# Kernel optimization log

Hardware: AMD Instinct MI355X
Metric: run time of the kernel (lower is better)

The kernel has to match this reference:

```python
import jax, jax.numpy as jnp
import numpy as np

HIDDEN = 512
HEADS = 8
LN_EPS = 1e-5


def setup_inputs() -> dict:
    key = jax.random.key(0)
    ks = jax.random.split(key, 10)
    n, bsz, h = 128, 4, HIDDEN
    state = jax.random.normal(ks[0], (n, n, bsz, h), dtype=jnp.float32)
    relation = jax.random.normal(ks[1], (n, n, bsz, h), dtype=jnp.float32)
    attn_mask = jnp.zeros((n, bsz, n), dtype=bool)  # key_padding_mask, True = pad
    std = 0.02
    Wq = jax.random.normal(ks[2], (h, h), dtype=jnp.float32) * std
    bq = jnp.zeros((h,), dtype=jnp.float32)
    Wk = jax.random.normal(ks[3], (h, h), dtype=jnp.float32) * std
    bk = jnp.zeros((h,), dtype=jnp.float32)
    Wp = jax.random.normal(ks[4], (h, 2 * h), dtype=jnp.float32) * std
    bp = jnp.zeros((h,), dtype=jnp.float32)
    gamma = jnp.ones((h,), dtype=jnp.float32)
    beta = jnp.zeros((h,), dtype=jnp.float32)
    return {"state": state, "relation": relation, "attn_mask": attn_mask, "n": n,
            "Wq": Wq, "bq": bq, "Wk": Wk, "bk": bk, "Wp": Wp, "bp": bp,
            "gamma": gamma, "beta": beta}


def reference(state, relation, attn_mask, n, Wq, bq, Wk, bk, Wp, bp, gamma, beta):
    # state, relation: [n, n, bsz, h]; attn_mask: [n, bsz, n] (True = pad key)
    h = state.shape[-1]
    dh = h // HEADS
    scale = dh ** -0.5
    # per-row self-attention weights (eval mode: attention dropout is identity)
    q = (jnp.einsum('itbh,oh->itbo', state, Wq) + bq) * scale
    k = jnp.einsum('isbh,oh->isbo', state, Wk) + bk
    qh = q.reshape(q.shape[0], q.shape[1], q.shape[2], HEADS, dh)
    kh = k.reshape(k.shape[0], k.shape[1], k.shape[2], HEADS, dh)
    scores = jnp.einsum('itbnd,isbnd->ibnts', qh, kh)  # [n, bsz, H, t, s]
    pad = attn_mask[:, :, None, None, :]               # [n, bsz, 1, 1, s]
    scores = jnp.where(pad, -jnp.inf, scores)
    probs = jax.nn.softmax(scores, axis=-1)
    w = probs.mean(axis=2)                             # avg over heads -> [n, bsz, t, s]
    # x[i,t,b] = sum_s w[i,b,t,s] * state[i,s,b]
    x = jnp.einsum('ibts,isbh->itbh', w, state)
    # rel_mix[i,t,b] = sum_s w[i,b,t,s] * relation[s,t,b]
    rel_mix = jnp.einsum('ibts,stbh->itbh', w, relation)
    cat = jnp.concatenate([x, rel_mix], axis=-1)       # [n, n, bsz, 2h]
    out = jax.nn.relu(jnp.einsum('itbc,hc->itbh', cat, Wp) + bp)
    # dropout is identity in eval mode; residual + layernorm
    y = state + out
    mu = y.mean(axis=-1, keepdims=True)
    var = y.var(axis=-1, keepdims=True)
    return gamma * (y - mu) * jax.lax.rsqrt(var + LN_EPS) + beta
```

## Files before the change

kernel.cpp:

```cpp
#include <hip/hip_runtime.h>

typedef unsigned short u16;
typedef __attribute__((ext_vector_type(4))) unsigned short u16x4;
typedef __attribute__((ext_vector_type(8))) unsigned short u16x8;
typedef __attribute__((ext_vector_type(8))) short bf16x8;
typedef __attribute__((ext_vector_type(4))) float f32x4;

__device__ __forceinline__ u16 f2bf(float f) {
  union { float f; unsigned u; } v; v.f = f;
  unsigned r = v.u + 0x7fffu + ((v.u >> 16) & 1u);
  return (u16)(r >> 16);
}
__device__ __forceinline__ float bf2f(u16 u) {
  union { unsigned u; float f; } v; v.u = ((unsigned)u) << 16;
  return v.f;
}
__device__ __forceinline__ void gload16(const void* g, void* l) {
  __builtin_amdgcn_global_load_lds(
      (const __attribute__((address_space(1))) unsigned int*)g,
      (__attribute__((address_space(3))) unsigned int*)l, 16, 0, 0);
}

__global__ __launch_bounds__(256) void k_prep(
    const float* __restrict__ Wq, const float* __restrict__ Wk,
    const float* __restrict__ bq, const float* __restrict__ bk,
    const float* __restrict__ Wp,
    u16* __restrict__ wqk, u16* __restrict__ wp, float* __restrict__ bqk) {
  int idx = blockIdx.x * 256 + threadIdx.x;
  if (idx < 524288) {
    int o = idx >> 9, hh = idx & 511;
    wqk[idx] = f2bf((o < 512) ? Wq[o * 512 + hh] * 0.125f : Wk[(o - 512) * 512 + hh]);
    wp[idx] = f2bf(Wp[idx]);
  }
  if (idx < 1024) bqk[idx] = (idx < 512) ? bq[idx] * 0.125f : bk[idx - 512];
}

__global__ __launch_bounds__(256) void k_transpose_state(
    const float* __restrict__ src, u16* __restrict__ dst, u16* __restrict__ stB) {
  const int i = blockIdx.z, b = blockIdx.y;
  const int s0 = (blockIdx.x & 1) * 64, h0 = (blockIdx.x >> 1) * 64;
  __shared__ u16 T[64][72];
  const int tid = threadIdx.x;
  const int ls = tid >> 4, lh = (tid & 15) * 4;
#pragma unroll
  for (int rr = 0; rr < 4; ++rr) {
    int s = rr * 16 + ls;
    size_t flat = ((size_t)(i * 128 + s0 + s) * 4 + b) * 512 + h0 + lh;
    f32x4 v = *(const f32x4*)&src[flat];
    u16x4 w4 = { f2bf(v.x), f2bf(v.y), f2bf(v.z), f2bf(v.w) };
    *(u16x4*)&T[s][lh] = w4;
    *(u16x4*)&stB[flat] = w4;
  }
  __syncthreads();
#pragma unroll
  for (int it = 0; it < 2; ++it) {
    int work = it * 256 + tid;
    int hh = work >> 3, sg = (work & 7) * 8;
    u16x8 o;
#pragma unroll
    for (int j = 0; j < 8; ++j) o[j] = T[sg + j][hh];
    *(u16x8*)&dst[((i * 4 + b) * 512 + h0 + hh) * 128 + s0 + sg] = o;
  }
}

__global__ __launch_bounds__(256) void k_transpose_rel(
    const float* __restrict__ src, u16* __restrict__ dst) {
  const int t = blockIdx.z, b = blockIdx.y;
  const int s0 = (blockIdx.x & 1) * 64, h0 = (blockIdx.x >> 1) * 64;
  __shared__ u16 T[64][72];
  const int tid = threadIdx.x;
  const int ls = tid >> 4, lh = (tid & 15) * 4;
#pragma unroll
  for (int rr = 0; rr < 4; ++rr) {
    int s = rr * 16 + ls;
    f32x4 v = *(const f32x4*)&src[(((s0 + s) * 128 + t) * 4 + b) * 512 + h0 + lh];
    u16x4 w4 = { f2bf(v.x), f2bf(v.y), f2bf(v.z), f2bf(v.w) };
    *(u16x4*)&T[s][lh] = w4;
  }
  __syncthreads();
#pragma unroll
  for (int it = 0; it < 2; ++it) {
    int work = it * 256 + tid;
    int hh = work >> 3, sg = (work & 7) * 8;
    u16x8 o;
#pragma unroll
    for (int j = 0; j < 8; ++j) o[j] = T[sg + j][hh];
    *(u16x8*)&dst[((t * 4 + b) * 512 + h0 + hh) * 128 + s0 + sg] = o;
  }
}

__global__ __launch_bounds__(256) void k_qkproj(
    const u16* __restrict__ stB, const u16* __restrict__ wqk,
    const float* __restrict__ bqk, u16* __restrict__ qk) {
  const int m0 = blockIdx.y * 128, n0 = blockIdx.x * 128;
  __shared__ u16 smem[17408];
  u16* As = smem;
  u16* Bs = smem + 8192;
  const int tid = threadIdx.x, lane = tid & 63, wid = tid >> 6;
  const int l15 = lane & 15, l4 = lane >> 4;
  const int wm = (wid >> 1) * 64, wn = (wid & 1) * 64;
  const int lr = lane >> 3, lc = (lane & 7) * 8;
  const f32x4 fz = {0.f, 0.f, 0.f, 0.f};
  f32x4 acc[4][4];
#pragma unroll
  for (int a = 0; a < 4; ++a)
#pragma unroll
    for (int c = 0; c < 4; ++c) acc[a][c] = fz;
  for (int k0 = 0; k0 < 512; k0 += 64) {
    if (k0) __syncthreads();
#pragma unroll
    for (int j = 0; j < 4; ++j) {
      int rb = wid * 32 + j * 8;
      gload16(&stB[(size_t)(m0 + rb + lr) * 512 + k0 + lc], &As[rb * 64]);
      gload16(&wqk[(size_t)(n0 + rb + lr) * 512 + k0 + lc], &Bs[rb * 64]);
    }
    __syncthreads();
#pragma unroll
    for (int kk = 0; kk < 64; kk += 32) {
      bf16x8 af[4], bfr[4];
#pragma unroll
      for (int mf = 0; mf < 4; ++mf)
        af[mf] = *(const bf16x8*)&As[(wm + mf * 16 + l15) * 64 + kk + l4 * 8];
#pragma unroll
      for (int nf = 0; nf < 4; ++nf)
        bfr[nf] = *(const bf16x8*)&Bs[(wn + nf * 16 + l15) * 64 + kk + l4 * 8];
#pragma unroll
      for (int mf = 0; mf < 4; ++mf)
#pragma unroll
        for (int nf = 0; nf < 4; ++nf)
          acc[mf][nf] = __builtin_amdgcn_mfma_f32_16x16x32_bf16(af[mf], bfr[nf], acc[mf][nf], 0, 0, 0);
    }
  }
  float bias[4];
#pragma unroll
  for (int nf = 0; nf < 4; ++nf) bias[nf] = bqk[n0 + wn + nf * 16 + l15];
  __syncthreads();
  u16* Cs = smem;
#pragma unroll
  for (int mf = 0; mf < 4; ++mf)
#pragma unroll
    for (int nf = 0; nf < 4; ++nf)
#pragma unroll
      for (int r = 0; r < 4; ++r)
        Cs[(wm + mf * 16 + l4 * 4 + r) * 136 + wn + nf * 16 + l15] =
            f2bf(acc[mf][nf][r] + bias[nf]);
  __syncthreads();
#pragma unroll
  for (int rr = 0; rr < 8; ++rr) {
    int row = rr * 16 + (tid >> 4), c8 = (tid & 15) * 8;
    *(u16x8*)&qk[(size_t)(m0 + row) * 1024 + n0 + c8] = *(const u16x8*)&Cs[row * 136 + c8];
  }
}

__global__ __launch_bounds__(256) void k_scores(
    const u16* __restrict__ qk, const unsigned char* __restrict__ mask,
    u16* __restrict__ wbuf) {
  const int i = blockIdx.x, b = blockIdx.y;
  __shared__ u16 smem[2 * 128 * 72];
  u16* qs = smem;
  u16* ks = smem + 128 * 72;
  const int tid = threadIdx.x, lane = tid & 63, wid = tid >> 6;
  const int l15 = lane & 15, l4 = lane >> 4;
  float wacc[2][8][4];
#pragma unroll
  for (int mf = 0; mf < 2; ++mf)
#pragma unroll
    for (int nf = 0; nf < 8; ++nf)
#pragma unroll
      for (int r = 0; r < 4; ++r) wacc[mf][nf][r] = 0.f;
  bool mk[8];
#pragma unroll
  for (int nf = 0; nf < 8; ++nf) mk[nf] = mask[i * 512 + b * 128 + nf * 16 + l15] != 0;
  const int arow = tid >> 3, acol = (tid & 7) * 8;
  const f32x4 fz = {0.f, 0.f, 0.f, 0.f};
  for (int h = 0; h < 8; ++h) {
    __syncthreads();
#pragma unroll
    for (int rr = 0; rr < 4; ++rr) {
      int row = rr * 32 + arow;
      int base = ((i * 128 + row) * 4 + b) * 1024 + h * 64 + acol;
      *(u16x8*)&qs[row * 72 + acol] = *(const u16x8*)&qk[base];
      *(u16x8*)&ks[row * 72 + acol] = *(const u16x8*)&qk[base + 512];
    }
    __syncthreads();
#pragma unroll
    for (int mf = 0; mf < 2; ++mf) {
      f32x4 sc[8];
#pragma unroll
      for (int nf = 0; nf < 8; ++nf) sc[nf] = fz;
#pragma unroll
      for (int kk = 0; kk < 64; kk += 32) {
        bf16x8 a = *(const bf16x8*)&qs[(wid * 32 + mf * 16 + l15) * 72 + kk + l4 * 8];
#pragma unroll
        for (int nf = 0; nf < 8; ++nf) {
          bf16x8 bb = *(const bf16x8*)&ks[(nf * 16 + l15) * 72 + kk + l4 * 8];
          sc[nf] = __builtin_amdgcn_mfma_f32_16x16x32_bf16(a, bb, sc[nf], 0, 0, 0);
        }
      }
#pragma unroll
      for (int r = 0; r < 4; ++r) {
        float mx = -3e38f;
#pragma unroll
        for (int nf = 0; nf < 8; ++nf) mx = fmaxf(mx, mk[nf] ? -3e38f : sc[nf][r]);
#pragma unroll
        for (int d = 1; d < 16; d <<= 1) mx = fmaxf(mx, __shfl_xor(mx, d, 64));
        float p[8], sum = 0.f;
#pragma unroll
        for (int nf = 0; nf < 8; ++nf) {
          p[nf] = mk[nf] ? 0.f : __expf(sc[nf][r] - mx);
          sum += p[nf];
        }
#pragma unroll
        for (int d = 1; d < 16; d <<= 1) sum += __shfl_xor(sum, d, 64);
        float inv = 0.125f / sum;
#pragma unroll
        for (int nf = 0; nf < 8; ++nf) wacc[mf][nf][r] += p[nf] * inv;
      }
    }
  }
#pragma unroll
  for (int mf = 0; mf < 2; ++mf)
#pragma unroll
    for (int nf = 0; nf < 8; ++nf)
#pragma unroll
      for (int r = 0; r < 4; ++r) {
        int t = wid * 32 + mf * 16 + l4 * 4 + r;
        wbuf[((i * 4 + b) * 128 + t) * 128 + nf * 16 + l15] = f2bf(wacc[mf][nf][r]);
      }
}

__global__ __launch_bounds__(256) void k_xmix(
    const u16* __restrict__ stT, const u16* __restrict__ wbuf,
    u16* __restrict__ xbuf) {
  const int i = blockIdx.x, b = blockIdx.y, hc = blockIdx.z;
  __shared__ u16 smem[2 * 128 * 136];
  u16* ST = smem;
  u16* WS = smem + 128 * 136;
  const int tid = threadIdx.x, lane = tid & 63, wid = tid >> 6;
  const int l15 = lane & 15, l4 = lane >> 4;
  const int wh = (wid >> 1) * 64, wt = (wid & 1) * 64;
  const f32x4 fz = {0.f, 0.f, 0.f, 0.f};
  f32x4 acc[4][4];
#pragma unroll
  for (int a = 0; a < 4; ++a)
#pragma unroll
    for (int c = 0; c < 4; ++c) acc[a][c] = fz;
  const int r16 = tid >> 4, c8 = (tid & 15) * 8;
#pragma unroll
  for (int rr = 0; rr < 8; ++rr) {
    int row = rr * 16 + r16;
    *(u16x8*)&ST[row * 136 + c8] =
        *(const u16x8*)&stT[((i * 4 + b) * 512 + hc * 128 + row) * 128 + c8];
    *(u16x8*)&WS[row * 136 + c8] =
        *(const u16x8*)&wbuf[((i * 4 + b) * 128 + row) * 128 + c8];
  }
  __syncthreads();
#pragma unroll
  for (int kk = 0; kk < 128; kk += 32) {
    bf16x8 af[4], bfr[4];
#pragma unroll
    for (int mf = 0; mf < 4; ++mf)
      af[mf] = *(const bf16x8*)&ST[(wh + mf * 16 + l15) * 136 + kk + l4 * 8];
#pragma unroll
    for (int nf = 0; nf < 4; ++nf)
      bfr[nf] = *(const bf16x8*)&WS[(wt + nf * 16 + l15) * 136 + kk + l4 * 8];
#pragma unroll
    for (int mf = 0; mf < 4; ++mf)
#pragma unroll
      for (int nf = 0; nf < 4; ++nf)
        acc[mf][nf] = __builtin_amdgcn_mfma_f32_16x16x32_bf16(af[mf], bfr[nf], acc[mf][nf], 0, 0, 0);
  }
  __syncthreads();
  u16* Cs = smem;
#pragma unroll
  for (int mf = 0; mf < 4; ++mf)
#pragma unroll
    for (int nf = 0; nf < 4; ++nf) {
      int h0 = wh + mf * 16 + l4 * 4;
      int t = wt + nf * 16 + l15;
      u16x4 pk = { f2bf(acc[mf][nf][0]), f2bf(acc[mf][nf][1]),
                   f2bf(acc[mf][nf][2]), f2bf(acc[mf][nf][3]) };
      *(u16x4*)&Cs[t * 136 + h0] = pk;
    }
  __syncthreads();
#pragma unroll
  for (int rr = 0; rr < 8; ++rr) {
    int t = rr * 16 + r16;
    *(u16x8*)&xbuf[((i * 128 + t) * 4 + b) * 512 + hc * 128 + c8] =
        *(const u16x8*)&Cs[t * 136 + c8];
  }
}

__global__ __launch_bounds__(256) void k_relmix(
    const u16* __restrict__ relT, const u16* __restrict__ wbuf,
    u16* __restrict__ relbuf) {
  const int t = blockIdx.x, b = blockIdx.y, hc = blockIdx.z;
  __shared__ u16 smem[2 * 128 * 136];
  u16* RT = smem;
  u16* WS = smem + 128 * 136;
  const int tid = threadIdx.x, lane = tid & 63, wid = tid >> 6;
  const int l15 = lane & 15, l4 = lane >> 4;
  const int wh = (wid >> 1) * 64, wi = (wid & 1) * 64;
  const f32x4 fz = {0.f, 0.f, 0.f, 0.f};
  f32x4 acc[4][4];
#pragma unroll
  for (int a = 0; a < 4; ++a)
#pragma unroll
    for (int c = 0; c < 4; ++c) acc[a][c] = fz;
  const int r16 = tid >> 4, c8 = (tid & 15) * 8;
#pragma unroll
  for (int rr = 0; rr < 8; ++rr) {
    int row = rr * 16 + r16;
    *(u16x8*)&RT[row * 136 + c8] =
        *(const u16x8*)&relT[((t * 4 + b) * 512 + hc * 128 + row) * 128 + c8];
    *(u16x8*)&WS[row * 136 + c8] =
        *(const u16x8*)&wbuf[((row * 4 + b) * 128 + t) * 128 + c8];
  }
  __syncthreads();
#pragma unroll
  for (int kk = 0; kk < 128; kk += 32) {
    bf16x8 af[4], bfr[4];
#pragma unroll
    for (int mf = 0; mf < 4; ++mf)
      af[mf] = *(const bf16x8*)&RT[(wh + mf * 16 + l15) * 136 + kk + l4 * 8];
#pragma unroll
    for (int nf = 0; nf < 4; ++nf)
      bfr[nf] = *(const bf16x8*)&WS[(wi + nf * 16 + l15) * 136 + kk + l4 * 8];
#pragma unroll
    for (int mf = 0; mf < 4; ++mf)
#pragma unroll
      for (int nf = 0; nf < 4; ++nf)
        acc[mf][nf] = __builtin_amdgcn_mfma_f32_16x16x32_bf16(af[mf], bfr[nf], acc[mf][nf], 0, 0, 0);
  }
  __syncthreads();
  u16* Cs = smem;
#pragma unroll
  for (int mf = 0; mf < 4; ++mf)
#pragma unroll
    for (int nf = 0; nf < 4; ++nf) {
      int h0 = wh + mf * 16 + l4 * 4;
      int ii = wi + nf * 16 + l15;
      u16x4 pk = { f2bf(acc[mf][nf][0]), f2bf(acc[mf][nf][1]),
                   f2bf(acc[mf][nf][2]), f2bf(acc[mf][nf][3]) };
      *(u16x4*)&Cs[ii * 136 + h0] = pk;
    }
  __syncthreads();
#pragma unroll
  for (int rr = 0; rr < 8; ++rr) {
    int ii = rr * 16 + r16;
    *(u16x8*)&relbuf[((ii * 128 + t) * 4 + b) * 512 + hc * 128 + c8] =
        *(const u16x8*)&Cs[ii * 136 + c8];
  }
}

__global__ __launch_bounds__(256) void k_proj(
    const u16* __restrict__ xbuf, const u16* __restrict__ relbuf,
    const u16* __restrict__ wp, const float* __restrict__ bp,
    u16* __restrict__ yb) {
  const int m0 = blockIdx.y * 128, n0 = blockIdx.x * 128;
  __shared__ u16 smem[17408];
  u16* As = smem;
  u16* Bs = smem + 8192;
  const int tid = threadIdx.x, lane = tid & 63, wid = tid >> 6;
  const int l15 = lane & 15, l4 = lane >> 4;
  const int wm = (wid >> 1) * 64, wn = (wid & 1) * 64;
  const int lr = lane >> 3, lc = (lane & 7) * 8;
  const f32x4 fz = {0.f, 0.f, 0.f, 0.f};
  f32x4 acc[4][4];
#pragma unroll
  for (int a = 0; a < 4; ++a)
#pragma unroll
    for (int c = 0; c < 4; ++c) acc[a][c] = fz;
  for (int k0 = 0; k0 < 1024; k0 += 64) {
    if (k0) __syncthreads();
    const u16* abase = (k0 < 512) ? xbuf + k0 : relbuf + (k0 - 512);
#pragma unroll
    for (int j = 0; j < 4; ++j) {
      int rb = wid * 32 + j * 8;
      gload16(&abase[(size_t)(m0 + rb + lr) * 512 + lc], &As[rb * 64]);
      gload16(&wp[(size_t)(n0 + rb + lr) * 1024 + k0 + lc], &Bs[rb * 64]);
    }
    __syncthreads();
#pragma unroll
    for (int kk = 0; kk < 64; kk += 32) {
      bf16x8 af[4], bfr[4];
#pragma unroll
      for (int mf = 0; mf < 4; ++mf)
        af[mf] = *(const bf16x8*)&As[(wm + mf * 16 + l15) * 64 + kk + l4 * 8];
#pragma unroll
      for (int nf = 0; nf < 4; ++nf)
        bfr[nf] = *(const bf16x8*)&Bs[(wn + nf * 16 + l15) * 64 + kk + l4 * 8];
#pragma unroll
      for (int mf = 0; mf < 4; ++mf)
#pragma unroll
        for (int nf = 0; nf < 4; ++nf)
          acc[mf][nf] = __builtin_amdgcn_mfma_f32_16x16x32_bf16(af[mf], bfr[nf], acc[mf][nf], 0, 0, 0);
    }
  }
  float bias[4];
#pragma unroll
  for (int nf = 0; nf < 4; ++nf) bias[nf] = bp[n0 + wn + nf * 16 + l15];
  __syncthreads();
  u16* Cs = smem;
#pragma unroll
  for (int mf = 0; mf < 4; ++mf)
#pragma unroll
    for (int nf = 0; nf < 4; ++nf)
#pragma unroll
      for (int r = 0; r < 4; ++r)
        Cs[(wm + mf * 16 + l4 * 4 + r) * 136 + wn + nf * 16 + l15] =
            f2bf(fmaxf(acc[mf][nf][r] + bias[nf], 0.f));
  __syncthreads();
#pragma unroll
  for (int rr = 0; rr < 8; ++rr) {
    int row = rr * 16 + (tid >> 4), c8 = (tid & 15) * 8;
    *(u16x8*)&yb[(size_t)(m0 + row) * 512 + n0 + c8] = *(const u16x8*)&Cs[row * 136 + c8];
  }
}

__global__ __launch_bounds__(256) void k_ln(
    const u16* __restrict__ yb, const float* __restrict__ state,
    const float* __restrict__ gamma, const float* __restrict__ beta,
    float* __restrict__ out) {
  const int tid = threadIdx.x, lane = tid & 63, wid = tid >> 6;
  f32x4 g0 = *(const f32x4*)&gamma[lane * 8];
  f32x4 g1 = *(const f32x4*)&gamma[lane * 8 + 4];
  f32x4 be0 = *(const f32x4*)&beta[lane * 8];
  f32x4 be1 = *(const f32x4*)&beta[lane * 8 + 4];
  for (int row = blockIdx.x * 4 + wid; row < 65536; row += gridDim.x * 4) {
    size_t gbase = (size_t)row * 512 + lane * 8;
    u16x8 yv = *(const u16x8*)&yb[gbase];
    f32x4 s0 = *(const f32x4*)&state[gbase];
    f32x4 s1 = *(const f32x4*)&state[gbase + 4];
    float y[8];
#pragma unroll
    for (int j = 0; j < 4; ++j) y[j] = bf2f(yv[j]) + s0[j];
#pragma unroll
    for (int j = 0; j < 4; ++j) y[4 + j] = bf2f(yv[4 + j]) + s1[j];
    float sum = 0.f, sq = 0.f;
#pragma unroll
    for (int j = 0; j < 8; ++j) { sum += y[j]; sq += y[j] * y[j]; }
#pragma unroll
    for (int d = 1; d < 64; d <<= 1) { sum += __shfl_xor(sum, d, 64); sq += __shfl_xor(sq, d, 64); }
    float mu = sum * (1.f / 512.f);
    float var = sq * (1.f / 512.f) - mu * mu;
    float rs = rsqrtf(var + 1e-5f);
    f32x4 o0, o1;
#pragma unroll
    for (int j = 0; j < 4; ++j) o0[j] = g0[j] * (y[j] - mu) * rs + be0[j];
#pragma unroll
    for (int j = 0; j < 4; ++j) o1[j] = g1[j] * (y[4 + j] - mu) * rs + be1[j];
    *(f32x4*)&out[gbase] = o0;
    *(f32x4*)&out[gbase + 4] = o1;
  }
}

extern "C" void kernel_launch(void* const* d_in, const int* in_sizes, int n_in,
                              void* d_out, int out_size, void* d_ws, size_t ws_size,
                              hipStream_t stream) {
  const float* state = (const float*)d_in[0];
  const float* relation = (const float*)d_in[1];
  const unsigned char* mask = (const unsigned char*)d_in[2];
  const float* Wq = (const float*)d_in[4];
  const float* bq = (const float*)d_in[5];
  const float* Wk = (const float*)d_in[6];
  const float* bk = (const float*)d_in[7];
  const float* Wp = (const float*)d_in[8];
  const float* bp = (const float*)d_in[9];
  const float* gamma = (const float*)d_in[10];
  const float* beta = (const float*)d_in[11];
  float* out = (float*)d_out;
  char* ws = (char*)d_ws;

  u16* qk     = (u16*)(ws);
  u16* xbuf   = (u16*)(ws);
  u16* relbuf = (u16*)(ws + 67108864);
  u16* stT    = (u16*)(ws + 134217728);
  u16* yb     = (u16*)(ws + 134217728);
  u16* relT   = (u16*)(ws + 201326592);
  u16* stB    = (u16*)(ws + 201326592);
  u16* wbuf   = (u16*)(ws + 268435456);
  u16* wqk    = (u16*)(ws + 285212672);
  u16* wp     = (u16*)(ws + 286261248);
  float* bqk  = (float*)(ws + 287309824);

  k_prep<<<2048, 256, 0, stream>>>(Wq, Wk, bq, bk, Wp, wqk, wp, bqk);
  k_transpose_state<<<dim3(16, 4, 128), 256, 0, stream>>>(state, stT, stB);
  k_qkproj<<<dim3(8, 512), 256, 0, stream>>>(stB, wqk, bqk, qk);
  k_scores<<<dim3(128, 4), 256, 0, stream>>>(qk, mask, wbuf);
  k_transpose_rel<<<dim3(16, 4, 128), 256, 0, stream>>>(relation, relT);
  k_xmix<<<dim3(128, 4, 4), 256, 0, stream>>>(stT, wbuf, xbuf);
  k_relmix<<<dim3(128, 4, 4), 256, 0, stream>>>(relT, wbuf, relbuf);
  k_proj<<<dim3(4, 512), 256, 0, stream>>>(xbuf, relbuf, wp, bp, yb);
  k_ln<<<2048, 256, 0, stream>>>(yb, state, gamma, beta, out);
}
```

Measured before the change: 466.0 us.

## Fuse relation transpose into relmix and remap GEMM blocks per XCD

Removes the separate relation transpose kernel. k_relmix now reads fp32 relation directly, converts it to bf16 and transposes it through shared memory in four chunks before running the MFMA. This drops a full bf16 write and read of the relation tensor and one launch, at the cost of more syncs and bank-conflicted LDS column reads inside relmix. The qkproj and proj GEMMs also switch to a 1D grid with an XCD-aware block mapping, so neighbouring M tiles land on the same XCD and can share L2.

```diff
diff --git a/kernel.cpp b/kernel.cpp
--- a/kernel.cpp
+++ b/kernel.cpp
@@ -14,6 +14,11 @@
 __device__ __forceinline__ float bf2f(u16 u) {
   union { unsigned u; float f; } v; v.u = ((unsigned)u) << 16;
   return v.f;
+}
+__device__ __forceinline__ u16x8 pack8(f32x4 a, f32x4 b) {
+  u16x8 r = { f2bf(a.x), f2bf(a.y), f2bf(a.z), f2bf(a.w),
+              f2bf(b.x), f2bf(b.y), f2bf(b.z), f2bf(b.w) };
+  return r;
 }
 __device__ __forceinline__ void gload16(const void* g, void* l) {
   __builtin_amdgcn_global_load_lds(
@@ -63,36 +68,13 @@
   }
 }
 
-__global__ __launch_bounds__(256) void k_transpose_rel(
-    const float* __restrict__ src, u16* __restrict__ dst) {
-  const int t = blockIdx.z, b = blockIdx.y;
-  const int s0 = (blockIdx.x & 1) * 64, h0 = (blockIdx.x >> 1) * 64;
-  __shared__ u16 T[64][72];
-  const int tid = threadIdx.x;
-  const int ls = tid >> 4, lh = (tid & 15) * 4;
-#pragma unroll
-  for (int rr = 0; rr < 4; ++rr) {
-    int s = rr * 16 + ls;
-    f32x4 v = *(const f32x4*)&src[(((s0 + s) * 128 + t) * 4 + b) * 512 + h0 + lh];
-    u16x4 w4 = { f2bf(v.x), f2bf(v.y), f2bf(v.z), f2bf(v.w) };
-    *(u16x4*)&T[s][lh] = w4;
-  }
-  __syncthreads();
-#pragma unroll
-  for (int it = 0; it < 2; ++it) {
-    int work = it * 256 + tid;
-    int hh = work >> 3, sg = (work & 7) * 8;
-    u16x8 o;
-#pragma unroll
-    for (int j = 0; j < 8; ++j) o[j] = T[sg + j][hh];
-    *(u16x8*)&dst[((t * 4 + b) * 512 + h0 + hh) * 128 + s0 + sg] = o;
-  }
-}
-
 __global__ __launch_bounds__(256) void k_qkproj(
     const u16* __restrict__ stB, const u16* __restrict__ wqk,
     const float* __restrict__ bqk, u16* __restrict__ qk) {
-  const int m0 = blockIdx.y * 128, n0 = blockIdx.x * 128;
+  const int flat = blockIdx.x;
+  const int xcd = flat & 7, local = flat >> 3;
+  const int m0 = (xcd * 64 + (local >> 3)) * 128;
+  const int n0 = (local & 7) * 128;
   __shared__ u16 smem[17408];
   u16* As = smem;
   u16* Bs = smem + 8192;
@@ -292,31 +274,53 @@
 }
 
 __global__ __launch_bounds__(256) void k_relmix(
-    const u16* __restrict__ relT, const u16* __restrict__ wbuf,
+    const float* __restrict__ relation, const u16* __restrict__ wbuf,
     u16* __restrict__ relbuf) {
   const int t = blockIdx.x, b = blockIdx.y, hc = blockIdx.z;
   __shared__ u16 smem[2 * 128 * 136];
   u16* RT = smem;
   u16* WS = smem + 128 * 136;
+  u16* T = WS;
   const int tid = threadIdx.x, lane = tid & 63, wid = tid >> 6;
   const int l15 = lane & 15, l4 = lane >> 4;
   const int wh = (wid >> 1) * 64, wi = (wid & 1) * 64;
+  const int sr = tid >> 3, hseg = (tid & 7) * 16;
+  const int th = tid >> 1, sseg = (tid & 1) * 16;
+#pragma unroll
+  for (int ch = 0; ch < 4; ++ch) {
+    const int sbase = ch * 32;
+    size_t gaddr = (((size_t)(sbase + sr) * 128 + t) * 4 + b) * 512 + hc * 128 + hseg;
+    f32x4 v0 = *(const f32x4*)&relation[gaddr];
+    f32x4 v1 = *(const f32x4*)&relation[gaddr + 4];
+    f32x4 v2 = *(const f32x4*)&relation[gaddr + 8];
+    f32x4 v3 = *(const f32x4*)&relation[gaddr + 12];
+    __syncthreads();
+    *(u16x8*)&T[sr * 136 + hseg] = pack8(v0, v1);
+    *(u16x8*)&T[sr * 136 + hseg + 8] = pack8(v2, v3);
+    __syncthreads();
+    u16x8 c0, c1;
+#pragma unroll
+    for (int j = 0; j < 8; ++j) c0[j] = T[(sseg + j) * 136 + th];
+#pragma unroll
+    for (int j = 0; j < 8; ++j) c1[j] = T[(sseg + 8 + j) * 136 + th];
+    *(u16x8*)&RT[th * 136 + sbase + sseg] = c0;
+    *(u16x8*)&RT[th * 136 + sbase + sseg + 8] = c1;
+  }
+  __syncthreads();
+  const int r16 = tid >> 4, c8 = (tid & 15) * 8;
+#pragma unroll
+  for (int rr = 0; rr < 8; ++rr) {
+    int row = rr * 16 + r16;
+    *(u16x8*)&WS[row * 136 + c8] =
+        *(const u16x8*)&wbuf[((row * 4 + b) * 128 + t) * 128 + c8];
+  }
+  __syncthreads();
   const f32x4 fz = {0.f, 0.f, 0.f, 0.f};
   f32x4 acc[4][4];
 #pragma unroll
   for (int a = 0; a < 4; ++a)
 #pragma unroll
     for (int c = 0; c < 4; ++c) acc[a][c] = fz;
-  const int r16 = tid >> 4, c8 = (tid & 15) * 8;
-#pragma unroll
-  for (int rr = 0; rr < 8; ++rr) {
-    int row = rr * 16 + r16;
-    *(u16x8*)&RT[row * 136 + c8] =
-        *(const u16x8*)&relT[((t * 4 + b) * 512 + hc * 128 + row) * 128 + c8];
-    *(u16x8*)&WS[row * 136 + c8] =
-        *(const u16x8*)&wbuf[((row * 4 + b) * 128 + t) * 128 + c8];
-  }
-  __syncthreads();
 #pragma unroll
   for (int kk = 0; kk < 128; kk += 32) {
     bf16x8 af[4], bfr[4];
@@ -357,7 +361,10 @@
     const u16* __restrict__ xbuf, const u16* __restrict__ relbuf,
     const u16* __restrict__ wp, const float* __restrict__ bp,
     u16* __restrict__ yb) {
-  const int m0 = blockIdx.y * 128, n0 = blockIdx.x * 128;
+  const int flat = blockIdx.x;
+  const int xcd = flat & 7, local = flat >> 3;
+  const int m0 = (xcd * 64 + (local >> 2)) * 128;
+  const int n0 = (local & 3) * 128;
   __shared__ u16 smem[17408];
   u16* As = smem;
   u16* Bs = smem + 8192;
@@ -477,7 +484,6 @@
   u16* relbuf = (u16*)(ws + 67108864);
   u16* stT    = (u16*)(ws + 134217728);
   u16* yb     = (u16*)(ws + 134217728);
-  u16* relT   = (u16*)(ws + 201326592);
   u16* stB    = (u16*)(ws + 201326592);
   u16* wbuf   = (u16*)(ws + 268435456);
   u16* wqk    = (u16*)(ws + 285212672);
@@ -486,11 +492,10 @@
 
   k_prep<<<2048, 256, 0, stream>>>(Wq, Wk, bq, bk, Wp, wqk, wp, bqk);
   k_transpose_state<<<dim3(16, 4, 128), 256, 0, stream>>>(state, stT, stB);
-  k_qkproj<<<dim3(8, 512), 256, 0, stream>>>(stB, wqk, bqk, qk);
+  k_qkproj<<<4096, 256, 0, stream>>>(stB, wqk, bqk, qk);
   k_scores<<<dim3(128, 4), 256, 0, stream>>>(qk, mask, wbuf);
-  k_transpose_rel<<<dim3(16, 4, 128), 256, 0, stream>>>(relation, relT);
   k_xmix<<<dim3(128, 4, 4), 256, 0, stream>>>(stT, wbuf, xbuf);
-  k_relmix<<<dim3(128, 4, 4), 256, 0, stream>>>(relT, wbuf, relbuf);
-  k_proj<<<dim3(4, 512), 256, 0, stream>>>(xbuf, relbuf, wp, bp, yb);
+  k_relmix<<<dim3(128, 4, 4), 256, 0, stream>>>(relation, wbuf, relbuf);
+  k_proj<<<2048, 256, 0, stream>>>(xbuf, relbuf, wp, bp, yb);
   k_ln<<<2048, 256, 0, stream>>>(yb, state, gamma, beta, out);
 }
```

Result: faster. 441.6 us (-5.2%).
